# Optimization experiments

Measured on AMD Instinct MI355X. Metric: run time of the kernel, lower is better.

## Reference

```python
import jax, jax.numpy as jnp
from jax import lax
import numpy as np

B, D, T, H = 256, 128, 1024, 64


def setup_inputs() -> dict:
    key = jax.random.key(0)
    ks = jax.random.split(key, 8)
    s = 1.0 / np.sqrt(H)
    latent_chunk = jax.random.normal(ks[0], (B, D, T), dtype=jnp.float32)
    hidden = jnp.zeros((1, B, H), dtype=jnp.float32)
    # PyTorch nn.GRU params: weight_ih [3H, D], weight_hh [3H, H], biases [3H]
    W_ih = jax.random.uniform(ks[1], (3 * H, D), minval=-s, maxval=s, dtype=jnp.float32)
    W_hh = jax.random.uniform(ks[2], (3 * H, H), minval=-s, maxval=s, dtype=jnp.float32)
    b_ih = jax.random.uniform(ks[3], (3 * H,), minval=-s, maxval=s, dtype=jnp.float32)
    b_hh = jax.random.uniform(ks[4], (3 * H,), minval=-s, maxval=s, dtype=jnp.float32)
    head_w = jax.random.uniform(ks[5], (1, H), minval=-s, maxval=s, dtype=jnp.float32)
    head_b = jax.random.uniform(ks[6], (1,), minval=-s, maxval=s, dtype=jnp.float32)
    return {"latent_chunk": latent_chunk, "hidden": hidden, "W_ih": W_ih,
            "W_hh": W_hh, "b_ih": b_ih, "b_hh": b_hh,
            "head_w": head_w, "head_b": head_b}


def _gru_forward(latent_chunk, hidden, W_ih, W_hh, b_ih, b_hh, head_w, head_b):
    # [B, D, T] -> [B, T, D]
    x = jnp.transpose(latent_chunk, (0, 2, 1))
    # Precompute input-gate projections once as a big GEMM: [B, T, 3H]
    xg = jnp.einsum('btd,gd->btg', x, W_ih) + b_ih
    xg_t = jnp.transpose(xg, (1, 0, 2))  # [T, B, 3H] for scan
    h0 = hidden[0]  # single layer: [B, H]

    def step(h, xg_step):
        hg = h @ W_hh.T + b_hh  # [B, 3H]
        xr, xz, xn = jnp.split(xg_step, 3, axis=-1)
        hr, hz, hn = jnp.split(hg, 3, axis=-1)
        r = jax.nn.sigmoid(xr + hr)
        z = jax.nn.sigmoid(xz + hz)
        n = jnp.tanh(xn + r * hn)
        h_new = (1.0 - z) * n + z * h
        return h_new, None

    hT, _ = lax.scan(step, h0, xg_t)
    # last output of single-layer GRU == final hidden state
    log_scale = hT @ head_w.T + head_b  # [B, 1]
    return log_scale, hT[None]  # hidden: [1, B, H]


def reference(latent_chunk, hidden, W_ih, W_hh, b_ih, b_hh, head_w, head_b):
    return _gru_forward(latent_chunk, hidden, W_ih, W_hh, b_ih, b_hh, head_w, head_b)
```

## Files before the change

kernel.cpp:

```cpp
#include <hip/hip_runtime.h>

#define B_ 256
#define D_ 128
#define T_ 1024
#define H_ 64
#define G_ 192
#define TILE_T 64
#define NTILES (T_ / TILE_T)
#define XGS 65
#define KC 32
#define WS 194

typedef float f32x4 __attribute__((ext_vector_type(4)));
typedef unsigned long long u64;

__global__ __launch_bounds__(448, 2) void gru_fused(
    const float* __restrict__ lat, const float* __restrict__ hidden_init,
    const float* __restrict__ W_ih, const float* __restrict__ W_hh,
    const float* __restrict__ b_ih, const float* __restrict__ b_hh,
    const float* __restrict__ head_w, const float* __restrict__ head_b,
    float* __restrict__ out)
{
    __shared__ float xg_s[2][G_ * XGS];
    __shared__ float lat_s[D_ * TILE_T];
    __shared__ float w_s[KC * WS];
    __shared__ float h_priv[3][H_];
    __shared__ u64  slot[3][2][H_];
    __shared__ unsigned prod_done[2], cons_done[2], pbar;

    const int b    = blockIdx.x;
    const int tid  = threadIdx.x;
    const int lane = tid & 63;
    const int wid  = tid >> 6;

    if (tid < 2) { prod_done[tid] = 0u; cons_done[tid] = 0u; }
    if (tid == 2) pbar = 0u;
    if (tid < 192) { slot[tid >> 6][0][tid & 63] = 0ull;
                     slot[tid >> 6][1][tid & 63] = 0ull; }
    __syncthreads();

    if (wid < 3) {
        __builtin_amdgcn_s_setprio(1);
        const int j   = lane;
        const int row = wid * H_ + j;
        f32x4 w4[16];
        {
            const f32x4* W = (const f32x4*)(W_hh + (size_t)row * H_);
#pragma unroll
            for (int q = 0; q < 16; ++q) w4[q] = W[q];
        }
        asm volatile("" : "+v"(w4[0]), "+v"(w4[1]), "+v"(w4[2]), "+v"(w4[3]),
                          "+v"(w4[4]), "+v"(w4[5]), "+v"(w4[6]), "+v"(w4[7]),
                          "+v"(w4[8]), "+v"(w4[9]), "+v"(w4[10]), "+v"(w4[11]),
                          "+v"(w4[12]), "+v"(w4[13]), "+v"(w4[14]), "+v"(w4[15]));
        const float bias = b_hh[row];
        const float hw   = (wid == 0) ? head_w[j] : 0.f;
        const int o1 = (wid == 0) ? 1 : 0;
        const int o2 = (wid == 2) ? 1 : 2;
        float h = hidden_init[b * H_ + j];
        unsigned sg = 0;

        for (int k = 0; k < NTILES; ++k) {
            const int s = k & 1;
            const unsigned tgt = 4u * (unsigned)((k >> 1) + 1);
            while (__hip_atomic_load(&prod_done[s], __ATOMIC_ACQUIRE,
                                     __HIP_MEMORY_SCOPE_WORKGROUP) < tgt)
                __builtin_amdgcn_s_sleep(1);
            const float* xr_p = &xg_s[s][(size_t)j * XGS];
            const float* xz_p = &xg_s[s][(size_t)(H_ + j) * XGS];
            const float* xn_p = &xg_s[s][(size_t)(2 * H_ + j) * XGS];

#pragma unroll 2
            for (int t = 0; t < TILE_T; ++t, ++sg) {
                const int par = (int)(sg & 1u);
                h_priv[wid][j] = h;
                float xr = xr_p[t], xz = xz_p[t], xn = xn_p[t];
                const f32x4* h4 = (const f32x4*)h_priv[wid];
                float a0 = 0.f, a1 = 0.f, a2 = 0.f, a3 = 0.f;
#pragma unroll
                for (int q = 0; q < 16; ++q) {
                    f32x4 hv = h4[q];
                    a0 = fmaf(w4[q].x, hv.x, a0); a1 = fmaf(w4[q].y, hv.y, a1);
                    a2 = fmaf(w4[q].z, hv.z, a2); a3 = fmaf(w4[q].w, hv.w, a3);
                }
                float a = ((a0 + a1) + (a2 + a3)) + bias;
                const unsigned want = sg + 1;

                u64 pk = ((u64)want << 32) | (u64)__builtin_bit_cast(unsigned, a);
                __hip_atomic_store(&slot[wid][par][j], pk, __ATOMIC_RELAXED,
                                   __HIP_MEMORY_SCOPE_WORKGROUP);
                u64 v1, v2;
                do {
                    v1 = __hip_atomic_load(&slot[o1][par][j], __ATOMIC_RELAXED,
                                           __HIP_MEMORY_SCOPE_WORKGROUP);
                    v2 = __hip_atomic_load(&slot[o2][par][j], __ATOMIC_RELAXED,
                                           __HIP_MEMORY_SCOPE_WORKGROUP);
                } while ((unsigned)(v1 >> 32) != want || (unsigned)(v2 >> 32) != want);
                float b1 = __builtin_bit_cast(float, (unsigned)v1);
                float b2 = __builtin_bit_cast(float, (unsigned)v2);

                float ar, az, an;
                if (wid == 0)      { ar = a;  az = b1; an = b2; }
                else if (wid == 1) { ar = b1; az = a;  an = b2; }
                else               { ar = b1; az = b2; an = a;  }

                float r   = __builtin_amdgcn_rcpf(1.f + __expf(-(xr + ar)));
                float z   = __builtin_amdgcn_rcpf(1.f + __expf(-(xz + az)));
                float pre = xn + r * an;
                float n   = fmaf(-2.f, __builtin_amdgcn_rcpf(__expf(2.f * pre) + 1.f), 1.f);
                h = fmaf(z, h - n, n);
            }
            if (lane == 0)
                __hip_atomic_fetch_add(&cons_done[s], 1u, __ATOMIC_RELEASE,
                                       __HIP_MEMORY_SCOPE_WORKGROUP);
        }

        if (wid == 0) {
            out[B_ + b * H_ + j] = h;
            float v = h * hw;
#pragma unroll
            for (int off = 32; off > 0; off >>= 1) v += __shfl_down(v, off);
            if (lane == 0) out[b] = v + head_b[0];
        }
    } else {
        const int p  = tid - 192;
        const int tx = p & 7;
        const int gy = p >> 3;
        const float* latb = lat + (size_t)b * (D_ * T_);
        unsigned phase = 0;

        auto psync = [&]() {
            if ((p & 63) == 0)
                __hip_atomic_fetch_add(&pbar, 1u, __ATOMIC_RELEASE,
                                       __HIP_MEMORY_SCOPE_WORKGROUP);
            ++phase;
            while (__hip_atomic_load(&pbar, __ATOMIC_ACQUIRE,
                                     __HIP_MEMORY_SCOPE_WORKGROUP) < 4u * phase) {}
        };

        float bias[6];
#pragma unroll
        for (int i = 0; i < 6; ++i) bias[i] = b_ih[gy * 6 + i];

        for (int k = 0; k < NTILES; ++k) {
            const int s = k & 1, m = k >> 1;
            if (m >= 1) {
                while (__hip_atomic_load(&cons_done[s], __ATOMIC_ACQUIRE,
                                         __HIP_MEMORY_SCOPE_WORKGROUP) < 3u * (unsigned)m)
                    __builtin_amdgcn_s_sleep(1);
            }
            psync();

#pragma unroll
            for (int i = 0; i < 32; ++i) {
                int f = p + 256 * i;
                int d = f >> 6, t = f & 63;
                lat_s[f] = latb[(size_t)d * T_ + k * TILE_T + t];
            }

            float acc[8][6];
#pragma unroll
            for (int jj = 0; jj < 8; ++jj)
#pragma unroll
                for (int i = 0; i < 6; ++i) acc[jj][i] = 0.f;

            for (int kc = 0; kc < D_; kc += KC) {
                psync();
#pragma unroll
                for (int i = 0; i < (G_ * KC) / 256; ++i) {
                    int f = p + 256 * i;
                    int g = f >> 5, kk = f & 31;
                    w_s[kk * WS + g] = W_ih[(size_t)g * D_ + kc + kk];
                }
                psync();
#pragma unroll 4
                for (int kk = 0; kk < KC; ++kk) {
                    f32x4 l0 = *(const f32x4*)&lat_s[(kc + kk) * 64 + tx * 8];
                    f32x4 l1 = *(const f32x4*)&lat_s[(kc + kk) * 64 + tx * 8 + 4];
                    float2 w0 = *(const float2*)&w_s[kk * WS + gy * 6];
                    float2 w1 = *(const float2*)&w_s[kk * WS + gy * 6 + 2];
                    float2 w2 = *(const float2*)&w_s[kk * WS + gy * 6 + 4];
                    float lv[8] = {l0.x, l0.y, l0.z, l0.w, l1.x, l1.y, l1.z, l1.w};
                    float wv[6] = {w0.x, w0.y, w1.x, w1.y, w2.x, w2.y};
#pragma unroll
                    for (int jj = 0; jj < 8; ++jj)
#pragma unroll
                        for (int i = 0; i < 6; ++i)
                            acc[jj][i] = fmaf(lv[jj], wv[i], acc[jj][i]);
                }
            }

            float* xs = xg_s[s];
#pragma unroll
            for (int i = 0; i < 6; ++i)
#pragma unroll
                for (int jj = 0; jj < 8; ++jj)
                    xs[(size_t)(gy * 6 + i) * XGS + tx * 8 + jj] = acc[jj][i] + bias[i];

            if ((p & 63) == 0)
                __hip_atomic_fetch_add(&prod_done[s], 1u, __ATOMIC_RELEASE,
                                       __HIP_MEMORY_SCOPE_WORKGROUP);
        }
    }
}

extern "C" void kernel_launch(void* const* d_in, const int* in_sizes, int n_in,
                              void* d_out, int out_size, void* d_ws, size_t ws_size,
                              hipStream_t stream)
{
    const float* lat   = (const float*)d_in[0];
    const float* hid0  = (const float*)d_in[1];
    const float* W_ih  = (const float*)d_in[2];
    const float* W_hh  = (const float*)d_in[3];
    const float* b_ih  = (const float*)d_in[4];
    const float* b_hh  = (const float*)d_in[5];
    const float* headw = (const float*)d_in[6];
    const float* headb = (const float*)d_in[7];
    float* out = (float*)d_out;

    gru_fused<<<dim3(B_), dim3(448), 0, stream>>>(
        lat, hid0, W_ih, W_hh, b_ih, b_hh, headw, headb, out);
}
```

Before: 454.3 us.

## Compute all three GRU gates in one wave, dropping cross-wave slot exchange

Replaces the three recurrent waves (one per gate) that traded gate pre-activations through versioned LDS slots with a single wave holding all three W_hh gate rows in registers. The per-timestep spin-wait handshake between waves goes away, and the block shrinks from 448 to 320 threads. In exchange each lane does three times the FMA work per step and needs about 192 VGPRs for weights, which raises register pressure on the serial critical path.

```diff
diff --git a/kernel.cpp b/kernel.cpp
--- a/kernel.cpp
+++ b/kernel.cpp
@@ -12,9 +12,9 @@
 #define WS 194
 
 typedef float f32x4 __attribute__((ext_vector_type(4)));
-typedef unsigned long long u64;
-
-__global__ __launch_bounds__(448, 2) void gru_fused(
+
+__global__ __attribute__((amdgpu_waves_per_eu(2, 2))) __launch_bounds__(320)
+void gru_fused(
     const float* __restrict__ lat, const float* __restrict__ hidden_init,
     const float* __restrict__ W_ih, const float* __restrict__ W_hh,
     const float* __restrict__ b_ih, const float* __restrict__ b_hh,
@@ -24,8 +24,7 @@
     __shared__ float xg_s[2][G_ * XGS];
     __shared__ float lat_s[D_ * TILE_T];
     __shared__ float w_s[KC * WS];
-    __shared__ float h_priv[3][H_];
-    __shared__ u64  slot[3][2][H_];
+    __shared__ float h_s[H_];
     __shared__ unsigned prod_done[2], cons_done[2], pbar;
 
     const int b    = blockIdx.x;
@@ -35,30 +34,34 @@
 
     if (tid < 2) { prod_done[tid] = 0u; cons_done[tid] = 0u; }
     if (tid == 2) pbar = 0u;
-    if (tid < 192) { slot[tid >> 6][0][tid & 63] = 0ull;
-                     slot[tid >> 6][1][tid & 63] = 0ull; }
     __syncthreads();
 
-    if (wid < 3) {
+    if (wid == 0) {
         __builtin_amdgcn_s_setprio(1);
-        const int j   = lane;
-        const int row = wid * H_ + j;
-        f32x4 w4[16];
+        const int j = lane;
+        f32x4 wr4[16], wz4[16], wn4[16];
         {
-            const f32x4* W = (const f32x4*)(W_hh + (size_t)row * H_);
-#pragma unroll
-            for (int q = 0; q < 16; ++q) w4[q] = W[q];
+            const f32x4* Wr = (const f32x4*)(W_hh + (size_t)j * H_);
+            const f32x4* Wz = (const f32x4*)(W_hh + (size_t)(H_ + j) * H_);
+            const f32x4* Wn = (const f32x4*)(W_hh + (size_t)(2 * H_ + j) * H_);
+#pragma unroll
+            for (int q = 0; q < 16; ++q) { wr4[q] = Wr[q]; wz4[q] = Wz[q]; wn4[q] = Wn[q]; }
         }
-        asm volatile("" : "+v"(w4[0]), "+v"(w4[1]), "+v"(w4[2]), "+v"(w4[3]),
-                          "+v"(w4[4]), "+v"(w4[5]), "+v"(w4[6]), "+v"(w4[7]),
-                          "+v"(w4[8]), "+v"(w4[9]), "+v"(w4[10]), "+v"(w4[11]),
-                          "+v"(w4[12]), "+v"(w4[13]), "+v"(w4[14]), "+v"(w4[15]));
-        const float bias = b_hh[row];
-        const float hw   = (wid == 0) ? head_w[j] : 0.f;
-        const int o1 = (wid == 0) ? 1 : 0;
-        const int o2 = (wid == 2) ? 1 : 2;
+        asm volatile("" : "+v"(wr4[0]), "+v"(wr4[1]), "+v"(wr4[2]), "+v"(wr4[3]),
+                          "+v"(wr4[4]), "+v"(wr4[5]), "+v"(wr4[6]), "+v"(wr4[7]),
+                          "+v"(wr4[8]), "+v"(wr4[9]), "+v"(wr4[10]), "+v"(wr4[11]),
+                          "+v"(wr4[12]), "+v"(wr4[13]), "+v"(wr4[14]), "+v"(wr4[15]));
+        asm volatile("" : "+v"(wz4[0]), "+v"(wz4[1]), "+v"(wz4[2]), "+v"(wz4[3]),
+                          "+v"(wz4[4]), "+v"(wz4[5]), "+v"(wz4[6]), "+v"(wz4[7]),
+                          "+v"(wz4[8]), "+v"(wz4[9]), "+v"(wz4[10]), "+v"(wz4[11]),
+                          "+v"(wz4[12]), "+v"(wz4[13]), "+v"(wz4[14]), "+v"(wz4[15]));
+        asm volatile("" : "+v"(wn4[0]), "+v"(wn4[1]), "+v"(wn4[2]), "+v"(wn4[3]),
+                          "+v"(wn4[4]), "+v"(wn4[5]), "+v"(wn4[6]), "+v"(wn4[7]),
+                          "+v"(wn4[8]), "+v"(wn4[9]), "+v"(wn4[10]), "+v"(wn4[11]),
+                          "+v"(wn4[12]), "+v"(wn4[13]), "+v"(wn4[14]), "+v"(wn4[15]));
+        const float br = b_hh[j], bz = b_hh[H_ + j], bn = b_hh[2 * H_ + j];
+        const float hw = head_w[j];
         float h = hidden_init[b * H_ + j];
-        unsigned sg = 0;
 
         for (int k = 0; k < NTILES; ++k) {
             const int s = k & 1;
@@ -71,38 +74,23 @@
             const float* xn_p = &xg_s[s][(size_t)(2 * H_ + j) * XGS];
 
 #pragma unroll 2
-            for (int t = 0; t < TILE_T; ++t, ++sg) {
-                const int par = (int)(sg & 1u);
-                h_priv[wid][j] = h;
+            for (int t = 0; t < TILE_T; ++t) {
+                h_s[j] = h;
                 float xr = xr_p[t], xz = xz_p[t], xn = xn_p[t];
-                const f32x4* h4 = (const f32x4*)h_priv[wid];
-                float a0 = 0.f, a1 = 0.f, a2 = 0.f, a3 = 0.f;
+                const f32x4* h4 = (const f32x4*)h_s;
+                f32x4 aR = {0.f, 0.f, 0.f, 0.f};
+                f32x4 aZ = {0.f, 0.f, 0.f, 0.f};
+                f32x4 aN = {0.f, 0.f, 0.f, 0.f};
 #pragma unroll
                 for (int q = 0; q < 16; ++q) {
                     f32x4 hv = h4[q];
-                    a0 = fmaf(w4[q].x, hv.x, a0); a1 = fmaf(w4[q].y, hv.y, a1);
-                    a2 = fmaf(w4[q].z, hv.z, a2); a3 = fmaf(w4[q].w, hv.w, a3);
+                    aR += wr4[q] * hv;
+                    aZ += wz4[q] * hv;
+                    aN += wn4[q] * hv;
                 }
-                float a = ((a0 + a1) + (a2 + a3)) + bias;
-                const unsigned want = sg + 1;
-
-                u64 pk = ((u64)want << 32) | (u64)__builtin_bit_cast(unsigned, a);
-                __hip_atomic_store(&slot[wid][par][j], pk, __ATOMIC_RELAXED,
-                                   __HIP_MEMORY_SCOPE_WORKGROUP);
-                u64 v1, v2;
-                do {
-                    v1 = __hip_atomic_load(&slot[o1][par][j], __ATOMIC_RELAXED,
-                                           __HIP_MEMORY_SCOPE_WORKGROUP);
-                    v2 = __hip_atomic_load(&slot[o2][par][j], __ATOMIC_RELAXED,
-                                           __HIP_MEMORY_SCOPE_WORKGROUP);
-                } while ((unsigned)(v1 >> 32) != want || (unsigned)(v2 >> 32) != want);
-                float b1 = __builtin_bit_cast(float, (unsigned)v1);
-                float b2 = __builtin_bit_cast(float, (unsigned)v2);
-
-                float ar, az, an;
-                if (wid == 0)      { ar = a;  az = b1; an = b2; }
-                else if (wid == 1) { ar = b1; az = a;  an = b2; }
-                else               { ar = b1; az = b2; an = a;  }
+                float ar = ((aR.x + aR.y) + (aR.z + aR.w)) + br;
+                float az = ((aZ.x + aZ.y) + (aZ.z + aZ.w)) + bz;
+                float an = ((aN.x + aN.y) + (aN.z + aN.w)) + bn;
 
                 float r   = __builtin_amdgcn_rcpf(1.f + __expf(-(xr + ar)));
                 float z   = __builtin_amdgcn_rcpf(1.f + __expf(-(xz + az)));
@@ -115,15 +103,13 @@
                                        __HIP_MEMORY_SCOPE_WORKGROUP);
         }
 
-        if (wid == 0) {
-            out[B_ + b * H_ + j] = h;
-            float v = h * hw;
-#pragma unroll
-            for (int off = 32; off > 0; off >>= 1) v += __shfl_down(v, off);
-            if (lane == 0) out[b] = v + head_b[0];
-        }
+        out[B_ + b * H_ + j] = h;
+        float v = h * hw;
+#pragma unroll
+        for (int off = 32; off > 0; off >>= 1) v += __shfl_down(v, off);
+        if (lane == 0) out[b] = v + head_b[0];
     } else {
-        const int p  = tid - 192;
+        const int p  = tid - 64;
         const int tx = p & 7;
         const int gy = p >> 3;
         const float* latb = lat + (size_t)b * (D_ * T_);
@@ -146,7 +132,7 @@
             const int s = k & 1, m = k >> 1;
             if (m >= 1) {
                 while (__hip_atomic_load(&cons_done[s], __ATOMIC_ACQUIRE,
-                                         __HIP_MEMORY_SCOPE_WORKGROUP) < 3u * (unsigned)m)
+                                         __HIP_MEMORY_SCOPE_WORKGROUP) < (unsigned)m)
                     __builtin_amdgcn_s_sleep(1);
             }
             psync();
@@ -218,6 +204,6 @@
     const float* headb = (const float*)d_in[7];
     float* out = (float*)d_out;
 
-    gru_fused<<<dim3(B_), dim3(448), 0, stream>>>(
+    gru_fused<<<dim3(B_), dim3(320), 0, stream>>>(
         lat, hid0, W_ih, W_hh, b_ih, b_hh, headw, headb, out);
 }
```

Measured after the change: 452.9 us. Within noise of the previous version (-0.3%).

## Replace atomic spin-wait handshakes with lockstep workgroup barriers and sliced producer schedule

Applied to the files above, without the earlier changes.

Replaces the per-step atomic slot polling and the producer/consumer counters with a single hardware s_barrier per recurrence step shared by all seven waves. The input-projection GEMM for the next tile is split into small per-step slices (global load, LDS store, 4-k FMA chunks, final write) so that it runs in lockstep with the recurrence, one tile ahead. This removes the spin loops and the 64-bit tagged packing, but it ties every step to the slowest wave, including the producer waves. Launch bounds drop the min-2-blocks hint and KC is halved to fit the slicing.

```diff
diff --git a/kernel.cpp b/kernel.cpp
--- a/kernel.cpp
+++ b/kernel.cpp
@@ -6,15 +6,14 @@
 #define H_ 64
 #define G_ 192
 #define TILE_T 64
-#define NTILES (T_ / TILE_T)
+#define NTILES 16
 #define XGS 65
-#define KC 32
+#define KC 16
 #define WS 194
 
 typedef float f32x4 __attribute__((ext_vector_type(4)));
-typedef unsigned long long u64;
-
-__global__ __launch_bounds__(448, 2) void gru_fused(
+
+__global__ __launch_bounds__(448) void gru_fused(
     const float* __restrict__ lat, const float* __restrict__ hidden_init,
     const float* __restrict__ W_ih, const float* __restrict__ W_hh,
     const float* __restrict__ b_ih, const float* __restrict__ b_hh,
@@ -25,19 +24,19 @@
     __shared__ float lat_s[D_ * TILE_T];
     __shared__ float w_s[KC * WS];
     __shared__ float h_priv[3][H_];
-    __shared__ u64  slot[3][2][H_];
-    __shared__ unsigned prod_done[2], cons_done[2], pbar;
+    __shared__ float slotv[2][3][H_];
 
     const int b    = blockIdx.x;
     const int tid  = threadIdx.x;
     const int lane = tid & 63;
     const int wid  = tid >> 6;
 
-    if (tid < 2) { prod_done[tid] = 0u; cons_done[tid] = 0u; }
-    if (tid == 2) pbar = 0u;
-    if (tid < 192) { slot[tid >> 6][0][tid & 63] = 0ull;
-                     slot[tid >> 6][1][tid & 63] = 0ull; }
-    __syncthreads();
+#define STEP_BARRIER() do {                                   \
+        __builtin_amdgcn_sched_barrier(0);                    \
+        asm volatile("s_waitcnt lgkmcnt(0)" ::: "memory");    \
+        __builtin_amdgcn_s_barrier();                         \
+        __builtin_amdgcn_sched_barrier(0);                    \
+    } while (0)
 
     if (wid < 3) {
         __builtin_amdgcn_s_setprio(1);
@@ -58,23 +57,18 @@
         const int o1 = (wid == 0) ? 1 : 0;
         const int o2 = (wid == 2) ? 1 : 2;
         float h = hidden_init[b * H_ + j];
-        unsigned sg = 0;
-
-        for (int k = 0; k < NTILES; ++k) {
-            const int s = k & 1;
-            const unsigned tgt = 4u * (unsigned)((k >> 1) + 1);
-            while (__hip_atomic_load(&prod_done[s], __ATOMIC_ACQUIRE,
-                                     __HIP_MEMORY_SCOPE_WORKGROUP) < tgt)
-                __builtin_amdgcn_s_sleep(1);
-            const float* xr_p = &xg_s[s][(size_t)j * XGS];
-            const float* xz_p = &xg_s[s][(size_t)(H_ + j) * XGS];
-            const float* xn_p = &xg_s[s][(size_t)(2 * H_ + j) * XGS];
-
-#pragma unroll 2
-            for (int t = 0; t < TILE_T; ++t, ++sg) {
-                const int par = (int)(sg & 1u);
-                h_priv[wid][j] = h;
-                float xr = xr_p[t], xz = xz_p[t], xn = xn_p[t];
+        h_priv[wid][j] = h;
+
+        for (int tt = 0; tt < (NTILES + 1) * TILE_T; ++tt) {
+            const int k  = (tt >> 6) - 1;
+            const int ph = tt & 63;
+            const int par = tt & 1;
+            float a = 0.f, xr = 0.f, xz = 0.f, xn = 0.f;
+            if (k >= 0) {
+                const int s = k & 1;
+                xr = xg_s[s][(size_t)j * XGS + ph];
+                xz = xg_s[s][(size_t)(H_ + j) * XGS + ph];
+                xn = xg_s[s][(size_t)(2 * H_ + j) * XGS + ph];
                 const f32x4* h4 = (const f32x4*)h_priv[wid];
                 float a0 = 0.f, a1 = 0.f, a2 = 0.f, a3 = 0.f;
 #pragma unroll
@@ -83,36 +77,27 @@
                     a0 = fmaf(w4[q].x, hv.x, a0); a1 = fmaf(w4[q].y, hv.y, a1);
                     a2 = fmaf(w4[q].z, hv.z, a2); a3 = fmaf(w4[q].w, hv.w, a3);
                 }
-                float a = ((a0 + a1) + (a2 + a3)) + bias;
-                const unsigned want = sg + 1;
-
-                u64 pk = ((u64)want << 32) | (u64)__builtin_bit_cast(unsigned, a);
-                __hip_atomic_store(&slot[wid][par][j], pk, __ATOMIC_RELAXED,
+                a = ((a0 + a1) + (a2 + a3)) + bias;
+                __hip_atomic_store(&slotv[par][wid][j], a, __ATOMIC_RELAXED,
                                    __HIP_MEMORY_SCOPE_WORKGROUP);
-                u64 v1, v2;
-                do {
-                    v1 = __hip_atomic_load(&slot[o1][par][j], __ATOMIC_RELAXED,
-                                           __HIP_MEMORY_SCOPE_WORKGROUP);
-                    v2 = __hip_atomic_load(&slot[o2][par][j], __ATOMIC_RELAXED,
-                                           __HIP_MEMORY_SCOPE_WORKGROUP);
-                } while ((unsigned)(v1 >> 32) != want || (unsigned)(v2 >> 32) != want);
-                float b1 = __builtin_bit_cast(float, (unsigned)v1);
-                float b2 = __builtin_bit_cast(float, (unsigned)v2);
-
+            }
+            STEP_BARRIER();
+            if (k >= 0) {
+                float b1 = __hip_atomic_load(&slotv[par][o1][j], __ATOMIC_RELAXED,
+                                             __HIP_MEMORY_SCOPE_WORKGROUP);
+                float b2 = __hip_atomic_load(&slotv[par][o2][j], __ATOMIC_RELAXED,
+                                             __HIP_MEMORY_SCOPE_WORKGROUP);
                 float ar, az, an;
                 if (wid == 0)      { ar = a;  az = b1; an = b2; }
                 else if (wid == 1) { ar = b1; az = a;  an = b2; }
                 else               { ar = b1; az = b2; an = a;  }
-
                 float r   = __builtin_amdgcn_rcpf(1.f + __expf(-(xr + ar)));
                 float z   = __builtin_amdgcn_rcpf(1.f + __expf(-(xz + az)));
                 float pre = xn + r * an;
                 float n   = fmaf(-2.f, __builtin_amdgcn_rcpf(__expf(2.f * pre) + 1.f), 1.f);
                 h = fmaf(z, h - n, n);
+                h_priv[wid][j] = h;
             }
-            if (lane == 0)
-                __hip_atomic_fetch_add(&cons_done[s], 1u, __ATOMIC_RELEASE,
-                                       __HIP_MEMORY_SCOPE_WORKGROUP);
         }
 
         if (wid == 0) {
@@ -127,81 +112,94 @@
         const int tx = p & 7;
         const int gy = p >> 3;
         const float* latb = lat + (size_t)b * (D_ * T_);
-        unsigned phase = 0;
-
-        auto psync = [&]() {
-            if ((p & 63) == 0)
-                __hip_atomic_fetch_add(&pbar, 1u, __ATOMIC_RELEASE,
-                                       __HIP_MEMORY_SCOPE_WORKGROUP);
-            ++phase;
-            while (__hip_atomic_load(&pbar, __ATOMIC_ACQUIRE,
-                                     __HIP_MEMORY_SCOPE_WORKGROUP) < 4u * phase) {}
-        };
 
         float bias[6];
 #pragma unroll
         for (int i = 0; i < 6; ++i) bias[i] = b_ih[gy * 6 + i];
 
-        for (int k = 0; k < NTILES; ++k) {
-            const int s = k & 1, m = k >> 1;
-            if (m >= 1) {
-                while (__hip_atomic_load(&cons_done[s], __ATOMIC_ACQUIRE,
-                                         __HIP_MEMORY_SCOPE_WORKGROUP) < 3u * (unsigned)m)
-                    __builtin_amdgcn_s_sleep(1);
-            }
-            psync();
-
-#pragma unroll
-            for (int i = 0; i < 32; ++i) {
-                int f = p + 256 * i;
-                int d = f >> 6, t = f & 63;
-                lat_s[f] = latb[(size_t)d * T_ + k * TILE_T + t];
-            }
-
-            float acc[8][6];
-#pragma unroll
-            for (int jj = 0; jj < 8; ++jj)
-#pragma unroll
-                for (int i = 0; i < 6; ++i) acc[jj][i] = 0.f;
-
-            for (int kc = 0; kc < D_; kc += KC) {
-                psync();
-#pragma unroll
-                for (int i = 0; i < (G_ * KC) / 256; ++i) {
-                    int f = p + 256 * i;
-                    int g = f >> 5, kk = f & 31;
-                    w_s[kk * WS + g] = W_ih[(size_t)g * D_ + kc + kk];
-                }
-                psync();
-#pragma unroll 4
-                for (int kk = 0; kk < KC; ++kk) {
-                    f32x4 l0 = *(const f32x4*)&lat_s[(kc + kk) * 64 + tx * 8];
-                    f32x4 l1 = *(const f32x4*)&lat_s[(kc + kk) * 64 + tx * 8 + 4];
-                    float2 w0 = *(const float2*)&w_s[kk * WS + gy * 6];
-                    float2 w1 = *(const float2*)&w_s[kk * WS + gy * 6 + 2];
-                    float2 w2 = *(const float2*)&w_s[kk * WS + gy * 6 + 4];
-                    float lv[8] = {l0.x, l0.y, l0.z, l0.w, l1.x, l1.y, l1.z, l1.w};
-                    float wv[6] = {w0.x, w0.y, w1.x, w1.y, w2.x, w2.y};
+        f32x4 latv[8];
+        float wreg[12];
+        float acc[8][6];
+#pragma unroll
+        for (int jj = 0; jj < 8; ++jj)
+#pragma unroll
+            for (int i = 0; i < 6; ++i) acc[jj][i] = 0.f;
+
+        for (int tt = 0; tt < (NTILES + 1) * TILE_T; ++tt) {
+            const int kp = tt >> 6;
+            const int ph = tt & 63;
+            if (kp <= NTILES - 1) {
+                if (ph == 0) {
+#pragma unroll
+                    for (int i = 0; i < 8; ++i) {
+                        int f4 = p + 256 * i;
+                        int d  = f4 >> 4;
+                        int t4 = (f4 & 15) * 4;
+                        latv[i] = *(const f32x4*)&latb[(size_t)d * T_ + kp * TILE_T + t4];
+                    }
+                } else if (ph == 6) {
+#pragma unroll
+                    for (int i = 0; i < 8; ++i) {
+                        int f4 = p + 256 * i;
+                        int d  = f4 >> 4;
+                        int t4 = (f4 & 15) * 4;
+                        *(f32x4*)&lat_s[d * 64 + t4] = latv[i];
+                    }
 #pragma unroll
                     for (int jj = 0; jj < 8; ++jj)
 #pragma unroll
-                        for (int i = 0; i < 6; ++i)
-                            acc[jj][i] = fmaf(lv[jj], wv[i], acc[jj][i]);
+                        for (int i = 0; i < 6; ++i) acc[jj][i] = 0.f;
+                } else if (ph >= 7 && ph <= 54) {
+                    const int q = ph - 7;
+                    const int c = q / 6;
+                    const int r = q - 6 * c;
+                    if (r == 0) {
+#pragma unroll
+                        for (int i = 0; i < 12; ++i) {
+                            int f = p + 256 * i;
+                            int g = f >> 4, kkl = f & 15;
+                            wreg[i] = W_ih[(size_t)g * D_ + c * KC + kkl];
+                        }
+                    } else if (r == 1) {
+#pragma unroll
+                        for (int i = 0; i < 12; ++i) {
+                            int f = p + 256 * i;
+                            int g = f >> 4, kkl = f & 15;
+                            w_s[kkl * WS + g] = wreg[i];
+                        }
+                    } else {
+#pragma unroll
+                        for (int u = 0; u < 4; ++u) {
+                            const int kkl = (r - 2) * 4 + u;
+                            const int kg  = c * KC + kkl;
+                            f32x4 l0 = *(const f32x4*)&lat_s[kg * 64 + tx * 8];
+                            f32x4 l1 = *(const f32x4*)&lat_s[kg * 64 + tx * 8 + 4];
+                            float2 w0 = *(const float2*)&w_s[kkl * WS + gy * 6];
+                            float2 w1 = *(const float2*)&w_s[kkl * WS + gy * 6 + 2];
+                            float2 w2 = *(const float2*)&w_s[kkl * WS + gy * 6 + 4];
+                            float lv[8] = {l0.x, l0.y, l0.z, l0.w, l1.x, l1.y, l1.z, l1.w};
+                            float wv[6] = {w0.x, w0.y, w1.x, w1.y, w2.x, w2.y};
+#pragma unroll
+                            for (int jj = 0; jj < 8; ++jj)
+#pragma unroll
+                                for (int i = 0; i < 6; ++i)
+                                    acc[jj][i] = fmaf(lv[jj], wv[i], acc[jj][i]);
+                        }
+                    }
+                } else if (ph == 55) {
+                    float* xs = xg_s[kp & 1];
+#pragma unroll
+                    for (int i = 0; i < 6; ++i)
+#pragma unroll
+                        for (int jj = 0; jj < 8; ++jj)
+                            xs[(size_t)(gy * 6 + i) * XGS + tx * 8 + jj] =
+                                acc[jj][i] + bias[i];
                 }
             }
-
-            float* xs = xg_s[s];
-#pragma unroll
-            for (int i = 0; i < 6; ++i)
-#pragma unroll
-                for (int jj = 0; jj < 8; ++jj)
-                    xs[(size_t)(gy * 6 + i) * XGS + tx * 8 + jj] = acc[jj][i] + bias[i];
-
-            if ((p & 63) == 0)
-                __hip_atomic_fetch_add(&prod_done[s], 1u, __ATOMIC_RELEASE,
-                                       __HIP_MEMORY_SCOPE_WORKGROUP);
+            STEP_BARRIER();
         }
     }
+#undef STEP_BARRIER
 }
 
 extern "C" void kernel_launch(void* const* d_in, const int* in_sizes, int n_in,
```

Result: slower. 988.0 us (+117.5%).
